# Performance work log

Measured on AMD Instinct MI355X. Metric: run time of the kernel, lower is better.

Reference implementation:

```python
import jax, jax.numpy as jnp
import numpy as np

B, S, D, H, DFF = 4, 2048, 1024, 16, 4096
DK = D // H
EPS = 1e-5


def _linear_params(key, fan_in, fan_out):
    kw, kb = jax.random.split(key)
    bound = 1.0 / np.sqrt(fan_in)
    w = jax.random.uniform(kw, (fan_in, fan_out), minval=-bound, maxval=bound, dtype=jnp.float32)
    b = jax.random.uniform(kb, (fan_out,), minval=-bound, maxval=bound, dtype=jnp.float32)
    return w, b


def setup_inputs() -> dict:
    key = jax.random.key(0)
    ks = jax.random.split(key, 8)
    x = jax.random.normal(ks[0], (B, S, D), dtype=jnp.float32)
    mask = jnp.ones((B, 1, 1, S), dtype=jnp.int32)
    wq, bq = _linear_params(ks[1], D, D)
    wk, bk = _linear_params(ks[2], D, D)
    wv, bv = _linear_params(ks[3], D, D)
    wo, bo = _linear_params(ks[4], D, D)
    w1, b1 = _linear_params(ks[5], D, DFF)
    w2, b2 = _linear_params(ks[6], DFF, D)
    g1 = jnp.ones((D,), jnp.float32); be1 = jnp.zeros((D,), jnp.float32)
    g2 = jnp.ones((D,), jnp.float32); be2 = jnp.zeros((D,), jnp.float32)
    return {"x": x, "mask": mask, "wq": wq, "bq": bq, "wk": wk, "bk": bk,
            "wv": wv, "bv": bv, "wo": wo, "bo": bo, "w1": w1, "b1": b1,
            "w2": w2, "b2": b2, "g1": g1, "be1": be1, "g2": g2, "be2": be2}


def _layernorm(x, g, b):
    mu = jnp.mean(x, axis=-1, keepdims=True)
    var = jnp.mean(jnp.square(x - mu), axis=-1, keepdims=True)
    return (x - mu) * jax.lax.rsqrt(var + EPS) * g + b


def reference(x, mask, wq, bq, wk, bk, wv, bv, wo, bo, w1, b1, w2, b2, g1, be1, g2, be2):
    # Multi-head self-attention
    q = (x @ wq + bq).reshape(B, S, H, DK).transpose(0, 2, 1, 3)  # b h s d
    k = (x @ wk + bk).reshape(B, S, H, DK).transpose(0, 2, 1, 3)
    v = (x @ wv + bv).reshape(B, S, H, DK).transpose(0, 2, 1, 3)
    scores = jnp.einsum('bhqd,bhkd->bhqk', q, k) / np.sqrt(DK)
    scores = jnp.where(mask == 0, jnp.float32(-1e9), scores)
    attn = jax.nn.softmax(scores, axis=-1)
    ctx = jnp.einsum('bhqk,bhkd->bhqd', attn, v)
    ctx = ctx.transpose(0, 2, 1, 3).reshape(B, S, D)
    attn_out = ctx @ wo + bo
    # Dropout is identity in eval mode
    out1 = _layernorm(x + attn_out, g1, be1)
    ffn = jax.nn.relu(out1 @ w1 + b1) @ w2 + b2
    out2 = _layernorm(out1 + ffn, g2, be2)
    return out2
```

## Files before the change

kernel.cpp:

```cpp
#include <hip/hip_runtime.h>
#include <cstdint>
#include <cstddef>

typedef __bf16 bf16_t;
typedef __bf16 bf16x4 __attribute__((ext_vector_type(4)));
typedef __bf16 bf16x8 __attribute__((ext_vector_type(8)));
typedef float f32x4 __attribute__((ext_vector_type(4)));

#define GLD_LDS16(g, l)                                                                   \
  __builtin_amdgcn_global_load_lds((const __attribute__((address_space(1))) void*)(g),   \
                                   (__attribute__((address_space(3))) void*)(l), 16, 0, 0)

__device__ __forceinline__ int swbits(int row) {
  return ((row ^ (row >> 3)) & 7) << 4;
}
__device__ __forceinline__ int swz(int row, int colbyte) {
  return row * 128 + (colbyte ^ swbits(row));
}

__global__ __launch_bounds__(256) void transpose_cvt_k(const float* __restrict__ src,
                                                       bf16_t* __restrict__ dst, int R, int C) {
  __shared__ float t[64][65];
  const int tid = threadIdx.x;
  const int tr = blockIdx.y * 64, tc = blockIdx.x * 64;
  const int r0 = tid >> 2, c0 = (tid & 3) * 16;
#pragma unroll
  for (int i = 0; i < 16; i += 4) {
    float4 v = *(const float4*)(src + (size_t)(tr + r0) * C + tc + c0 + i);
    t[r0][c0 + i] = v.x; t[r0][c0 + i + 1] = v.y;
    t[r0][c0 + i + 2] = v.z; t[r0][c0 + i + 3] = v.w;
  }
  __syncthreads();
  bf16x8 w0, w1;
#pragma unroll
  for (int i = 0; i < 8; ++i) {
    w0[i] = (bf16_t)t[c0 + i][r0];
    w1[i] = (bf16_t)t[c0 + 8 + i][r0];
  }
  *(bf16x8*)(dst + (size_t)(tc + r0) * R + tr + c0) = w0;
  *(bf16x8*)(dst + (size_t)(tc + r0) * R + tr + c0 + 8) = w1;
}

__global__ __launch_bounds__(256) void cvt_k(const float* __restrict__ in,
                                             bf16_t* __restrict__ out) {
  const size_t i = ((size_t)blockIdx.x * 256 + threadIdx.x) * 8;
  float4 a = *(const float4*)(in + i);
  float4 b = *(const float4*)(in + i + 4);
  bf16x8 o;
  o[0] = (bf16_t)a.x; o[1] = (bf16_t)a.y; o[2] = (bf16_t)a.z; o[3] = (bf16_t)a.w;
  o[4] = (bf16_t)b.x; o[5] = (bf16_t)b.y; o[6] = (bf16_t)b.z; o[7] = (bf16_t)b.w;
  *(bf16x8*)(out + i) = o;
}

template <int EPI>
__global__ __launch_bounds__(256) void gemm_bt(
    const bf16_t* __restrict__ A, const bf16_t* __restrict__ Bt,
    const float* __restrict__ bias0, const float* __restrict__ bias1,
    const float* __restrict__ bias2, const bf16_t* __restrict__ res,
    bf16_t* __restrict__ out0, bf16_t* __restrict__ out1, bf16_t* __restrict__ out2,
    int N, int K) {
  __shared__ __align__(16) bf16_t As[128][64];
  __shared__ __align__(16) bf16_t Bs[128][64];
  const int tid = threadIdx.x, lane = tid & 63, wave = tid >> 6;
  const int wm = wave >> 1, wn = wave & 1;
  const int tile_m = blockIdx.y * 128, tile_n = blockIdx.x * 128;

  f32x4 acc[4][4];
#pragma unroll
  for (int i = 0; i < 4; ++i)
#pragma unroll
    for (int j = 0; j < 4; ++j)
#pragma unroll
      for (int c = 0; c < 4; ++c) acc[i][j][c] = 0.f;

  for (int k0 = 0; k0 < K; k0 += 64) {
    __syncthreads();
#pragma unroll
    for (int j = 0; j < 4; ++j) {
      const int c = j * 256 + tid;
      GLD_LDS16(A + (size_t)(tile_m + (c >> 3)) * K + k0 + (c & 7) * 8,
                (char*)As + j * 4096 + wave * 1024);
      GLD_LDS16(Bt + (size_t)(tile_n + (c >> 3)) * K + k0 + (c & 7) * 8,
                (char*)Bs + j * 4096 + wave * 1024);
    }
    __syncthreads();
#pragma unroll
    for (int kk = 0; kk < 2; ++kk) {
      bf16x8 a[4], b[4];
#pragma unroll
      for (int i = 0; i < 4; ++i)
        a[i] = *(const bf16x8*)&As[wm * 64 + i * 16 + (lane & 15)][kk * 32 + (lane >> 4) * 8];
#pragma unroll
      for (int i = 0; i < 4; ++i)
        b[i] = *(const bf16x8*)&Bs[wn * 64 + i * 16 + (lane & 15)][kk * 32 + (lane >> 4) * 8];
#pragma unroll
      for (int mi = 0; mi < 4; ++mi)
#pragma unroll
        for (int ni = 0; ni < 4; ++ni)
          acc[mi][ni] = __builtin_amdgcn_mfma_f32_16x16x32_bf16(a[mi], b[ni], acc[mi][ni], 0, 0, 0);
    }
  }

#pragma unroll
  for (int mi = 0; mi < 4; ++mi) {
#pragma unroll
    for (int ni = 0; ni < 4; ++ni) {
      const int col = tile_n + wn * 64 + ni * 16 + (lane & 15);
      const int rbase = tile_m + wm * 64 + mi * 16 + (lane >> 4) * 4;
      if constexpr (EPI == 0) {
        const int which = col >> 10, cc = col & 1023;
        const float* bp = which == 0 ? bias0 : (which == 1 ? bias1 : bias2);
        bf16_t* op = which == 0 ? out0 : (which == 1 ? out1 : out2);
        const float bv = bp[cc];
        const float sca = which == 0 ? 0.18033688f : 1.0f;
        const int h = cc >> 6, dk = cc & 63;
#pragma unroll
        for (int r = 0; r < 4; ++r) {
          const int row = rbase + r, bb = row >> 11, ss = row & 2047;
          op[(((size_t)bb * 16 + h) * 2048 + ss) * 64 + dk] = (bf16_t)((acc[mi][ni][r] + bv) * sca);
        }
      } else {
        const float bv = bias0[col];
#pragma unroll
        for (int r = 0; r < 4; ++r) {
          const int row = rbase + r;
          float v = acc[mi][ni][r] + bv;
          if constexpr (EPI == 1) v += (float)res[(size_t)row * N + col];
          if constexpr (EPI == 2) v = v > 0.f ? v : 0.f;
          out0[(size_t)row * N + col] = (bf16_t)v;
        }
      }
    }
  }
}

__global__ __launch_bounds__(256) void attn_k(
    const bf16_t* __restrict__ Q, const bf16_t* __restrict__ Kb, const bf16_t* __restrict__ Vb,
    const int* __restrict__ mask, bf16_t* __restrict__ ctxout) {
  __shared__ __align__(16) char Qs[16384];
  __shared__ __align__(16) char Ks[2][8192];
  __shared__ __align__(16) char Vt[2][8192];
  __shared__ __align__(16) char Ps[16384];
  const int tid = threadIdx.x, lane = tid & 63, wave = tid >> 6;
  const int fr = lane & 15, hi = lane >> 4;
  const int qt = blockIdx.x, bh = blockIdx.y, b = bh >> 4, h = bh & 15;
  const bf16_t* qbase = Q + ((size_t)bh * 2048 + qt * 128) * 64;
  const bf16_t* kbase = Kb + (size_t)bh * 2048 * 64;
  const bf16_t* vbase = Vb + (size_t)bh * 2048 * 64;
  const int* mbase = mask + b * 2048;

  const int src_r = tid >> 3;
  const int src_cb = (tid & 7) * 16;

#pragma unroll
  for (int j = 0; j < 4; ++j) {
    const int c = j * 256 + tid, rr = c >> 3, cb = (c & 7) * 16;
    GLD_LDS16(qbase + rr * 64 + ((cb ^ swbits(rr)) >> 1), Qs + j * 4096 + wave * 1024);
  }
#pragma unroll
  for (int j = 0; j < 2; ++j) {
    const int rr = j * 32 + src_r;
    GLD_LDS16(kbase + rr * 64 + ((src_cb ^ swbits(rr)) >> 1), Ks[0] + j * 4096 + wave * 1024);
  }
  {
    bf16x8 v0 = *(const bf16x8*)(vbase + (size_t)(tid >> 3) * 64 + (tid & 7) * 8);
    bf16x8 v1 = *(const bf16x8*)(vbase + (size_t)(32 + (tid >> 3)) * 64 + (tid & 7) * 8);
    const int kp0 = tid >> 3, kp1 = 32 + (tid >> 3), d0 = (tid & 7) * 8;
#pragma unroll
    for (int i = 0; i < 8; ++i) {
      *(bf16_t*)(Vt[0] + swz(d0 + i, kp0 * 2)) = v0[i];
      *(bf16_t*)(Vt[0] + swz(d0 + i, kp1 * 2)) = v1[i];
    }
  }
  __syncthreads();

  f32x4 ctx[2][4];
  float l_prt[2][4];
#pragma unroll
  for (int mi = 0; mi < 2; ++mi)
#pragma unroll
    for (int r = 0; r < 4; ++r) {
      l_prt[mi][r] = 0.f;
#pragma unroll
      for (int di = 0; di < 4; ++di) ctx[mi][di][r] = 0.f;
    }

  for (int kt = 0; kt < 32; ++kt) {
    const int cur = kt & 1;
    bf16x8 vr0, vr1;
    if (kt < 31) {
#pragma unroll
      for (int j = 0; j < 2; ++j) {
        const int rr = j * 32 + src_r;
        GLD_LDS16(kbase + (size_t)(kt + 1) * 4096 + rr * 64 + ((src_cb ^ swbits(rr)) >> 1),
                  Ks[cur ^ 1] + j * 4096 + wave * 1024);
      }
      vr0 = *(const bf16x8*)(vbase + (size_t)(kt + 1) * 4096 + (size_t)(tid >> 3) * 64 +
                             (tid & 7) * 8);
      vr1 = *(const bf16x8*)(vbase + (size_t)(kt + 1) * 4096 + (size_t)(32 + (tid >> 3)) * 64 +
                             (tid & 7) * 8);
    }
    int mv[4];
#pragma unroll
    for (int ni = 0; ni < 4; ++ni) mv[ni] = mbase[kt * 64 + ni * 16 + fr];

    f32x4 sc[2][4];
#pragma unroll
    for (int mi = 0; mi < 2; ++mi)
#pragma unroll
      for (int ni = 0; ni < 4; ++ni)
#pragma unroll
        for (int c = 0; c < 4; ++c) sc[mi][ni][c] = 0.f;
#pragma unroll
    for (int kk = 0; kk < 2; ++kk) {
      bf16x8 aq[2], kb_[4];
#pragma unroll
      for (int mi = 0; mi < 2; ++mi)
        aq[mi] = *(const bf16x8*)(Qs + swz(wave * 32 + mi * 16 + fr, kk * 64 + hi * 16));
#pragma unroll
      for (int ni = 0; ni < 4; ++ni)
        kb_[ni] = *(const bf16x8*)(Ks[cur] + swz(ni * 16 + fr, kk * 64 + hi * 16));
#pragma unroll
      for (int mi = 0; mi < 2; ++mi)
#pragma unroll
        for (int ni = 0; ni < 4; ++ni)
          sc[mi][ni] = __builtin_amdgcn_mfma_f32_16x16x32_bf16(aq[mi], kb_[ni], sc[mi][ni], 0, 0, 0);
    }

#pragma unroll
    for (int mi = 0; mi < 2; ++mi) {
#pragma unroll
      for (int r = 0; r < 4; ++r) {
        float rsum = 0.f;
#pragma unroll
        for (int ni = 0; ni < 4; ++ni) {
          const float p = mv[ni] ? exp2f(sc[mi][ni][r]) : 0.f;
          sc[mi][ni][r] = p;
          rsum += p;
        }
        l_prt[mi][r] += rsum;
      }
      const int qrow = wave * 32 + mi * 16 + hi * 4;
#pragma unroll
      for (int ni = 0; ni < 4; ++ni)
#pragma unroll
        for (int r = 0; r < 4; ++r)
          *(bf16_t*)(Ps + swz(qrow + r, (ni * 16 + fr) * 2)) = (bf16_t)sc[mi][ni][r];
    }
    asm volatile("s_waitcnt lgkmcnt(0)" ::: "memory");
    __builtin_amdgcn_sched_barrier(0);

#pragma unroll
    for (int kk = 0; kk < 2; ++kk) {
      bf16x8 pa[2], vv[4];
#pragma unroll
      for (int mi = 0; mi < 2; ++mi)
        pa[mi] = *(const bf16x8*)(Ps + swz(wave * 32 + mi * 16 + fr, kk * 64 + hi * 16));
#pragma unroll
      for (int di = 0; di < 4; ++di)
        vv[di] = *(const bf16x8*)(Vt[cur] + swz(di * 16 + fr, kk * 64 + hi * 16));
#pragma unroll
      for (int mi = 0; mi < 2; ++mi)
#pragma unroll
        for (int di = 0; di < 4; ++di)
          ctx[mi][di] =
              __builtin_amdgcn_mfma_f32_16x16x32_bf16(pa[mi], vv[di], ctx[mi][di], 0, 0, 0);
    }

    if (kt < 31) {
      const int kp0 = tid >> 3, kp1 = 32 + (tid >> 3), d0 = (tid & 7) * 8;
#pragma unroll
      for (int i = 0; i < 8; ++i) {
        *(bf16_t*)(Vt[cur ^ 1] + swz(d0 + i, kp0 * 2)) = vr0[i];
        *(bf16_t*)(Vt[cur ^ 1] + swz(d0 + i, kp1 * 2)) = vr1[i];
      }
    }
    __syncthreads();
  }

#pragma unroll
  for (int mi = 0; mi < 2; ++mi)
#pragma unroll
    for (int r = 0; r < 4; ++r) {
      float l = l_prt[mi][r];
#pragma unroll
      for (int d = 1; d < 16; d <<= 1) l += __shfl_xor(l, d);
      const float inv = 1.f / l;
      const int srow = qt * 128 + wave * 32 + mi * 16 + hi * 4 + r;
#pragma unroll
      for (int di = 0; di < 4; ++di) {
        const int col = h * 64 + di * 16 + fr;
        ctxout[((size_t)b * 2048 + srow) * 1024 + col] = (bf16_t)(ctx[mi][di][r] * inv);
      }
    }
}

template <int F32OUT>
__global__ __launch_bounds__(256) void ln_k(const bf16_t* __restrict__ in,
                                            const float* __restrict__ g,
                                            const float* __restrict__ be,
                                            void* __restrict__ out) {
  __shared__ float red[8];
  const int tid = threadIdx.x;
  const size_t row = blockIdx.x;
  bf16x4 v4 = *(const bf16x4*)(in + row * 1024 + tid * 4);
  const float f0 = (float)v4[0], f1 = (float)v4[1], f2 = (float)v4[2], f3 = (float)v4[3];
  float s = f0 + f1 + f2 + f3;
  float s2 = f0 * f0 + f1 * f1 + f2 * f2 + f3 * f3;
#pragma unroll
  for (int d = 1; d < 64; d <<= 1) { s += __shfl_xor(s, d); s2 += __shfl_xor(s2, d); }
  if ((tid & 63) == 0) { red[tid >> 6] = s; red[4 + (tid >> 6)] = s2; }
  __syncthreads();
  s = red[0] + red[1] + red[2] + red[3];
  s2 = red[4] + red[5] + red[6] + red[7];
  const float mu = s * (1.f / 1024.f);
  const float var = s2 * (1.f / 1024.f) - mu * mu;
  const float rs = rsqrtf(var + 1e-5f);
  float4 gv = *(const float4*)(g + tid * 4);
  float4 bv = *(const float4*)(be + tid * 4);
  const float r0 = (f0 - mu) * rs * gv.x + bv.x;
  const float r1 = (f1 - mu) * rs * gv.y + bv.y;
  const float r2 = (f2 - mu) * rs * gv.z + bv.z;
  const float r3 = (f3 - mu) * rs * gv.w + bv.w;
  if constexpr (F32OUT) {
    float4 o = {r0, r1, r2, r3};
    *(float4*)((float*)out + row * 1024 + tid * 4) = o;
  } else {
    bf16x4 o;
    o[0] = (bf16_t)r0; o[1] = (bf16_t)r1; o[2] = (bf16_t)r2; o[3] = (bf16_t)r3;
    *(bf16x4*)((bf16_t*)out + row * 1024 + tid * 4) = o;
  }
}

extern "C" void kernel_launch(void* const* d_in, const int* in_sizes, int n_in,
                              void* d_out, int out_size, void* d_ws, size_t ws_size,
                              hipStream_t stream) {
  const float* x    = (const float*)d_in[0];
  const int*   mask = (const int*)d_in[1];
  const float* wq = (const float*)d_in[2];
  const float* bq = (const float*)d_in[3];
  const float* wk = (const float*)d_in[4];
  const float* bk = (const float*)d_in[5];
  const float* wv = (const float*)d_in[6];
  const float* bv = (const float*)d_in[7];
  const float* wo = (const float*)d_in[8];
  const float* bo = (const float*)d_in[9];
  const float* w1 = (const float*)d_in[10];
  const float* b1 = (const float*)d_in[11];
  const float* w2 = (const float*)d_in[12];
  const float* b2 = (const float*)d_in[13];
  const float* g1  = (const float*)d_in[14];
  const float* be1 = (const float*)d_in[15];
  const float* g2  = (const float*)d_in[16];
  const float* be2 = (const float*)d_in[17];

  char* wsb = (char*)d_ws;
  bf16_t* S0  = (bf16_t*)wsb;
  bf16_t* XB  = (bf16_t*)(wsb + 8388608);
  bf16_t* QB  = (bf16_t*)(wsb + 25165824);
  bf16_t* KB  = (bf16_t*)(wsb + 41943040);
  bf16_t* VB  = (bf16_t*)(wsb + 58720256);
  bf16_t* CTX = (bf16_t*)(wsb + 75497472);
  bf16_t* FFN = QB;
  bf16_t* Y   = (bf16_t*)(wsb + 92274688);
  bf16_t* O1  = (bf16_t*)(wsb + 109051904);

  dim3 blk(256);
  cvt_k<<<4096, blk, 0, stream>>>(x, XB);
  transpose_cvt_k<<<dim3(16, 16), blk, 0, stream>>>(wq, S0, 1024, 1024);
  transpose_cvt_k<<<dim3(16, 16), blk, 0, stream>>>(wk, S0 + 1048576, 1024, 1024);
  transpose_cvt_k<<<dim3(16, 16), blk, 0, stream>>>(wv, S0 + 2097152, 1024, 1024);
  gemm_bt<0><<<dim3(24, 64), blk, 0, stream>>>(XB, S0, bq, bk, bv, nullptr,
                                               QB, KB, VB, 3072, 1024);
  transpose_cvt_k<<<dim3(16, 16), blk, 0, stream>>>(wo, S0, 1024, 1024);
  attn_k<<<dim3(16, 64), blk, 0, stream>>>(QB, KB, VB, mask, CTX);
  gemm_bt<1><<<dim3(8, 64), blk, 0, stream>>>(CTX, S0, bo, nullptr, nullptr, XB,
                                              Y, nullptr, nullptr, 1024, 1024);
  transpose_cvt_k<<<dim3(64, 16), blk, 0, stream>>>(w1, S0, 1024, 4096);
  ln_k<0><<<8192, blk, 0, stream>>>(Y, g1, be1, O1);
  gemm_bt<2><<<dim3(32, 64), blk, 0, stream>>>(O1, S0, b1, nullptr, nullptr, nullptr,
                                               FFN, nullptr, nullptr, 4096, 1024);
  transpose_cvt_k<<<dim3(16, 64), blk, 0, stream>>>(w2, S0, 4096, 1024);
  gemm_bt<1><<<dim3(8, 64), blk, 0, stream>>>(FFN, S0, b2, nullptr, nullptr, O1,
                                              Y, nullptr, nullptr, 1024, 4096);
  ln_k<1><<<8192, blk, 0, stream>>>(Y, g2, be2, d_out);
}
```

Measured before the change: 512.8 us.

## Add 256x256-tile double-buffered GEMM for QKV and FFN1 projections

Adds a new 512-thread GEMM kernel with 256x256 output tiles. It double-buffers 128KB of dynamic LDS, filled by direct global-to-LDS loads into a swizzled layout, and uses barrier/setprio scheduling around the MFMA blocks. The QKV projection and the first FFN GEMM now use it. The larger tiles raise arithmetic intensity and cut operand reloads, and prefetching the next K-slice overlaps memory with compute. In exchange, occupancy is one block per CU, and the grids are small (384 and 512 blocks), which risks tail imbalance across the CUs.

```diff
diff --git a/kernel.cpp b/kernel.cpp
--- a/kernel.cpp
+++ b/kernel.cpp
@@ -55,10 +55,8 @@
 template <int EPI>
 __global__ __launch_bounds__(256) void gemm_bt(
     const bf16_t* __restrict__ A, const bf16_t* __restrict__ Bt,
-    const float* __restrict__ bias0, const float* __restrict__ bias1,
-    const float* __restrict__ bias2, const bf16_t* __restrict__ res,
-    bf16_t* __restrict__ out0, bf16_t* __restrict__ out1, bf16_t* __restrict__ out2,
-    int N, int K) {
+    const float* __restrict__ bias0, const bf16_t* __restrict__ res,
+    bf16_t* __restrict__ out0, int N, int K) {
   __shared__ __align__(16) bf16_t As[128][64];
   __shared__ __align__(16) bf16_t Bs[128][64];
   const int tid = threadIdx.x, lane = tid & 63, wave = tid >> 6;
@@ -107,25 +105,128 @@
     for (int ni = 0; ni < 4; ++ni) {
       const int col = tile_n + wn * 64 + ni * 16 + (lane & 15);
       const int rbase = tile_m + wm * 64 + mi * 16 + (lane >> 4) * 4;
+      const float bv = bias0[col];
+#pragma unroll
+      for (int r = 0; r < 4; ++r) {
+        const int row = rbase + r;
+        float v = acc[mi][ni][r] + bv;
+        if constexpr (EPI == 1) v += (float)res[(size_t)row * N + col];
+        out0[(size_t)row * N + col] = (bf16_t)v;
+      }
+    }
+  }
+}
+
+template <int EPI>
+__global__ __launch_bounds__(512, 1) void gemm256(
+    const bf16_t* __restrict__ A, const bf16_t* __restrict__ Bt,
+    const float* __restrict__ bias0, const float* __restrict__ bias1,
+    const float* __restrict__ bias2,
+    bf16_t* __restrict__ out0, bf16_t* __restrict__ out1, bf16_t* __restrict__ out2,
+    int N, int K) {
+  extern __shared__ __align__(16) char lds[];
+  const int tid = threadIdx.x, lane = tid & 63, wave = tid >> 6;
+  const int fr = lane & 15, hi = lane >> 4;
+  const int wm = wave >> 2, wn = wave & 3;
+  const int tile_n = blockIdx.x * 256, tile_m = blockIdx.y * 256;
+  const int NT = K >> 6;
+  const int s_r = tid >> 3, s_cb = (tid & 7) * 16;
+
+  f32x4 acc[8][4];
+#pragma unroll
+  for (int m = 0; m < 8; ++m)
+#pragma unroll
+    for (int n = 0; n < 4; ++n)
+#pragma unroll
+      for (int c = 0; c < 4; ++c) acc[m][n][c] = 0.f;
+
+#define STAGE256(t, cbuf)                                                                  \
+  do {                                                                                     \
+    const size_t k0_ = (size_t)(t) * 64;                                                   \
+    _Pragma("unroll") for (int h_ = 0; h_ < 2; ++h_)                                       \
+        _Pragma("unroll") for (int is_ = 0; is_ < 2; ++is_) {                              \
+      const int r_ = is_ * 64 + s_r;                                                       \
+      GLD_LDS16(A + (size_t)(tile_m + h_ * 128 + r_) * K + k0_ + ((s_cb ^ swbits(r_)) >> 1),\
+                lds + (cbuf)*65536 + h_ * 16384 + is_ * 8192 + wave * 1024);               \
+    }                                                                                      \
+    _Pragma("unroll") for (int h_ = 0; h_ < 2; ++h_)                                       \
+        _Pragma("unroll") for (int is_ = 0; is_ < 2; ++is_) {                              \
+      const int r_ = is_ * 64 + s_r;                                                       \
+      GLD_LDS16(Bt + (size_t)(tile_n + h_ * 128 + r_) * K + k0_ + ((s_cb ^ swbits(r_)) >> 1),\
+                lds + (cbuf)*65536 + 32768 + h_ * 16384 + is_ * 8192 + wave * 1024);       \
+    }                                                                                      \
+  } while (0)
+
+  STAGE256(0, 0);
+  for (int t = 0; t < NT; ++t) {
+    const int c = t & 1;
+    if (t + 1 < NT) {
+      STAGE256(t + 1, c ^ 1);
+      asm volatile("s_waitcnt vmcnt(8)" ::: "memory");
+    } else {
+      asm volatile("s_waitcnt vmcnt(0)" ::: "memory");
+    }
+    __builtin_amdgcn_s_barrier();
+    __builtin_amdgcn_sched_barrier(0);
+
+    bf16x8 bfrag[4][2];
+#pragma unroll
+    for (int n = 0; n < 4; ++n)
+#pragma unroll
+      for (int kk = 0; kk < 2; ++kk)
+        bfrag[n][kk] = *(const bf16x8*)(lds + c * 65536 + 32768 + (wn >> 1) * 16384 +
+                                        swz((wn & 1) * 64 + n * 16 + fr, kk * 64 + hi * 16));
+#pragma unroll
+    for (int p = 0; p < 4; ++p) {
+      bf16x8 afrag[2][2];
+#pragma unroll
+      for (int mm = 0; mm < 2; ++mm)
+#pragma unroll
+        for (int kk = 0; kk < 2; ++kk)
+          afrag[mm][kk] = *(const bf16x8*)(lds + c * 65536 + wm * 16384 +
+                                           swz((p * 2 + mm) * 16 + fr, kk * 64 + hi * 16));
+      __builtin_amdgcn_sched_barrier(0);
+      __builtin_amdgcn_s_barrier();
+      __builtin_amdgcn_s_setprio(1);
+#pragma unroll
+      for (int mm = 0; mm < 2; ++mm)
+#pragma unroll
+        for (int n = 0; n < 4; ++n)
+#pragma unroll
+          for (int kk = 0; kk < 2; ++kk)
+            acc[p * 2 + mm][n] = __builtin_amdgcn_mfma_f32_16x16x32_bf16(
+                afrag[mm][kk], bfrag[n][kk], acc[p * 2 + mm][n], 0, 0, 0);
+      __builtin_amdgcn_s_setprio(0);
+      __builtin_amdgcn_s_barrier();
+      __builtin_amdgcn_sched_barrier(0);
+    }
+  }
+#undef STAGE256
+
+#pragma unroll
+  for (int m = 0; m < 8; ++m) {
+#pragma unroll
+    for (int n = 0; n < 4; ++n) {
+      const int col = tile_n + wn * 64 + n * 16 + fr;
+      const int rbase = tile_m + wm * 128 + m * 16 + hi * 4;
       if constexpr (EPI == 0) {
-        const int which = col >> 10, cc = col & 1023;
+        const int which = tile_n >> 10;
         const float* bp = which == 0 ? bias0 : (which == 1 ? bias1 : bias2);
         bf16_t* op = which == 0 ? out0 : (which == 1 ? out1 : out2);
+        const float sca = which == 0 ? 0.18033688f : 1.0f;
+        const int cc = col & 1023, h = cc >> 6, dk = cc & 63;
         const float bv = bp[cc];
-        const float sca = which == 0 ? 0.18033688f : 1.0f;
-        const int h = cc >> 6, dk = cc & 63;
 #pragma unroll
         for (int r = 0; r < 4; ++r) {
           const int row = rbase + r, bb = row >> 11, ss = row & 2047;
-          op[(((size_t)bb * 16 + h) * 2048 + ss) * 64 + dk] = (bf16_t)((acc[mi][ni][r] + bv) * sca);
+          op[(((size_t)bb * 16 + h) * 2048 + ss) * 64 + dk] = (bf16_t)((acc[m][n][r] + bv) * sca);
         }
       } else {
         const float bv = bias0[col];
 #pragma unroll
         for (int r = 0; r < 4; ++r) {
           const int row = rbase + r;
-          float v = acc[mi][ni][r] + bv;
-          if constexpr (EPI == 1) v += (float)res[(size_t)row * N + col];
+          float v = acc[m][n][r] + bv;
           if constexpr (EPI == 2) v = v > 0.f ? v : 0.f;
           out0[(size_t)row * N + col] = (bf16_t)v;
         }
@@ -365,23 +466,26 @@
   bf16_t* Y   = (bf16_t*)(wsb + 92274688);
   bf16_t* O1  = (bf16_t*)(wsb + 109051904);
 
+  (void)hipFuncSetAttribute((const void*)gemm256<0>,
+                            hipFuncAttributeMaxDynamicSharedMemorySize, 131072);
+  (void)hipFuncSetAttribute((const void*)gemm256<2>,
+                            hipFuncAttributeMaxDynamicSharedMemorySize, 131072);
+
   dim3 blk(256);
   cvt_k<<<4096, blk, 0, stream>>>(x, XB);
   transpose_cvt_k<<<dim3(16, 16), blk, 0, stream>>>(wq, S0, 1024, 1024);
   transpose_cvt_k<<<dim3(16, 16), blk, 0, stream>>>(wk, S0 + 1048576, 1024, 1024);
   transpose_cvt_k<<<dim3(16, 16), blk, 0, stream>>>(wv, S0 + 2097152, 1024, 1024);
-  gemm_bt<0><<<dim3(24, 64), blk, 0, stream>>>(XB, S0, bq, bk, bv, nullptr,
-                                               QB, KB, VB, 3072, 1024);
+  gemm256<0><<<dim3(12, 32), 512, 131072, stream>>>(XB, S0, bq, bk, bv,
+                                                    QB, KB, VB, 3072, 1024);
   transpose_cvt_k<<<dim3(16, 16), blk, 0, stream>>>(wo, S0, 1024, 1024);
   attn_k<<<dim3(16, 64), blk, 0, stream>>>(QB, KB, VB, mask, CTX);
-  gemm_bt<1><<<dim3(8, 64), blk, 0, stream>>>(CTX, S0, bo, nullptr, nullptr, XB,
-                                              Y, nullptr, nullptr, 1024, 1024);
+  gemm_bt<1><<<dim3(8, 64), blk, 0, stream>>>(CTX, S0, bo, XB, Y, 1024, 1024);
   transpose_cvt_k<<<dim3(64, 16), blk, 0, stream>>>(w1, S0, 1024, 4096);
   ln_k<0><<<8192, blk, 0, stream>>>(Y, g1, be1, O1);
-  gemm_bt<2><<<dim3(32, 64), blk, 0, stream>>>(O1, S0, b1, nullptr, nullptr, nullptr,
-                                               FFN, nullptr, nullptr, 4096, 1024);
+  gemm256<2><<<dim3(16, 32), 512, 131072, stream>>>(O1, S0, b1, nullptr, nullptr,
+                                                    FFN, nullptr, nullptr, 4096, 1024);
   transpose_cvt_k<<<dim3(16, 64), blk, 0, stream>>>(w2, S0, 4096, 1024);
-  gemm_bt<1><<<dim3(8, 64), blk, 0, stream>>>(FFN, S0, b2, nullptr, nullptr, O1,
-                                              Y, nullptr, nullptr, 1024, 4096);
+  gemm_bt<1><<<dim3(8, 64), blk, 0, stream>>>(FFN, S0, b2, O1, Y, 1024, 4096);
   ln_k<1><<<8192, blk, 0, stream>>>(Y, g2, be2, d_out);
 }
```

Result: faster. 498.7 us (-2.8%).
